# Performance work log

Hardware: AMD Instinct MI355X
Metric: run time of the kernel (lower is better)

The kernel has to match this reference:

```python
import jax, jax.numpy as jnp
import numpy as np

N, D, E = 16384, 256, 131072  # nodes, feature dim, directed edges (avg sym degree ~16)


def _build_graph(rng):
    # random edges with no self-loops
    r = rng.integers(0, N, E)
    c = (r + 1 + rng.integers(0, N - 1, E)) % N
    e = np.stack([r, c], 1)
    # symmetrize + dedupe + sort == torch sparse coalesce()
    e = np.unique(np.concatenate([e, e[:, ::-1]], 0), axis=0)
    rows, cols = e[:, 0], e[:, 1]
    deg = np.bincount(rows, minlength=N)
    max_deg = int(deg.max())
    off = np.concatenate([[0], np.cumsum(deg)])
    pos = np.arange(rows.shape[0]) - off[rows]
    nbr = np.zeros((N, max_deg), dtype=np.int32)  # padded neighbor lists (CSR rows)
    nbr[rows, pos] = cols
    return nbr, deg.astype(np.int32)


def setup_inputs() -> dict:
    rng = np.random.default_rng(0)
    vertices = jnp.asarray(rng.standard_normal((N, D)).astype(np.float32))
    nbr, deg = _build_graph(rng)
    return {"vertices": vertices, "nbr": jnp.asarray(nbr), "deg": jnp.asarray(deg)}


def _compute_means(vertices, nbr, deg):
    # Sequential greedy edge-based vertex averaging (RelEdgePool phase 1).
    n, d = vertices.shape
    max_deg = nbr.shape[1]
    slot = jnp.arange(max_deg)

    def step(carry, xs):
        unproc, out, c = carry
        i, nbrs_i, deg_i = xs
        valid = slot < deg_i                      # real (non-pad) neighbors
        sel = valid & unproc[nbrs_i]              # unprocessed cluster members (excl. self)
        is_head = unproc[i]                       # vertex starts a new valid cluster
        # mean over unprocessed members; self is always included when head
        s = jnp.einsum('kd,k->d', vertices[nbrs_i], sel.astype(vertices.dtype)) + vertices[i]
        cnt = (jnp.sum(sel) + 1).astype(vertices.dtype)
        mean = s / cnt
        out = out.at[c].set(jnp.where(is_head, mean, out[c]))
        # mark selected members (and self) as processed, only if this is a head
        mark = jnp.zeros(n, bool).at[nbrs_i].max(sel).at[i].set(True)
        unproc = unproc & ~(mark & is_head)
        c = c + is_head.astype(c.dtype)
        return (unproc, out, c), is_head

    init = (jnp.ones(n, dtype=bool), jnp.zeros((n, d), vertices.dtype), jnp.int32(0))
    (_, out, num_clusters), head_mask = jax.lax.scan(
        step, init, (jnp.arange(n), nbr, deg))
    # out[:num_clusters] are the averaged vertices; rows beyond are zero (preallocated buffer,
    # matching the torch code before its final data-dependent slice).
    # head_mask marks vertex_mappings; mean_mappings == arange(num_clusters).
    return out, head_mask, num_clusters


def reference(vertices, nbr, deg):
    return _compute_means(vertices, nbr, deg)
```

## Files before the change

kernel.cpp:

```cpp
#include <hip/hip_runtime.h>
#include <cstdint>
#include <cstddef>

#define NV 16384
#define DD 256
#define BLK 1024
#define PCAP 7
#define HROW 24

__global__ __launch_bounds__(256)
void k_prep(const int* __restrict__ nbr, const int* __restrict__ deg,
            int maxdeg, int n, uint4* __restrict__ pend_g,
            unsigned short* __restrict__ hi_g)
{
    int v = blockIdx.x * 256 + threadIdx.x;
    if (v >= n) return;
    const int b  = v & ~(BLK - 1);
    const int dv = deg[v];
    const int* __restrict__ row = nbr + (size_t)v * (size_t)maxdeg;
    unsigned short* __restrict__ hrow = hi_g + (size_t)v * HROW;
    unsigned w0 = 0, w1 = 0, w2 = 0, w3 = 0;
    int cnt = 0, hic = 0;
    for (int k = 0; k < dv; ++k) {
        int j = row[k];
        if (j > v) {
            if (hic < HROW - 1) hrow[1 + hic] = (unsigned short)j;
            ++hic;
        } else if (j >= b) {
            unsigned val = (unsigned)(j - b);
            switch (cnt) {
                case 0: w0 |= val << 16; break;
                case 1: w1 |= val;       break;
                case 2: w1 |= val << 16; break;
                case 3: w2 |= val;       break;
                case 4: w2 |= val << 16; break;
                case 5: w3 |= val;       break;
                case 6: w3 |= val << 16; break;
                default: break;
            }
            ++cnt;
        }
    }
    hrow[0] = (unsigned short)hic;
    w0 |= (unsigned)(cnt > 0xffff ? 0xffff : cnt);
    uint4 p; p.x = w0; p.y = w1; p.z = w2; p.w = w3;
    pend_g[v] = p;
}

__global__ __launch_bounds__(1024)
void k_mis(const int* __restrict__ nbr, const int* __restrict__ deg,
           int maxdeg, int n,
           const uint4* __restrict__ pend_g, const unsigned short* __restrict__ hi_g,
           int* __restrict__ headlist, float* __restrict__ out_tail)
{
    __shared__ __align__(16) unsigned char st[NV];
    __shared__ int s_ws[16];
    __shared__ int F[3];
    const int t    = threadIdx.x;
    const int lane = t & 63;
    const int wid  = t >> 6;

    ((uint4*)st)[t] = make_uint4(0u, 0u, 0u, 0u);
    if (t < 3) F[t] = 0;
    __syncthreads();

    uint4 pv = make_uint4(0,0,0,0), h0 = pv, h1 = pv, h2 = pv;
    int   dv = 0;
    if (t < n) {
        pv = pend_g[t];
        const uint4* hp = (const uint4*)(hi_g + (size_t)t * HROW);
        h0 = hp[0]; h1 = hp[1]; h2 = hp[2];
        dv = deg[t];
    }
    int r = 0;

    for (int b = 0; b < n; b += BLK) {
        const int v = b + t;
        uint4 pn = make_uint4(0,0,0,0), n0 = pn, n1 = pn, n2 = pn;
        int   dn = 0;
        {
            int vn = b + BLK + t;
            if (vn < n) {
                pn = pend_g[vn];
                const uint4* hp = (const uint4*)(hi_g + (size_t)vn * HROW);
                n0 = hp[0]; n1 = hp[1]; n2 = hp[2];
                dn = deg[vn];
            }
        }

        const int np = pv.x & 0xffff;
        const int e0 = pv.x >> 16,    e1 = pv.y & 0xffff, e2 = pv.y >> 16;
        const int e3 = pv.z & 0xffff, e4 = pv.z >> 16;
        const int e5 = pv.w & 0xffff, e6 = pv.w >> 16;
        const int hic = (int)(h0.x & 0xffff);
        const int* __restrict__ row = nbr + (size_t)v * (size_t)maxdeg;

        int my = (v < n) ? 0 : 2;
        for (;; ++r) {
            if (t == 0) F[(r + 1) % 3] = 0;
            #pragma unroll
            for (int pass = 0; pass < 3; ++pass) {
                if (my == 0) {
                    if (st[v] != 0) { my = 2; }
                    else {
                        bool anyH = false; int undec = 0;
                        if (np <= PCAP) {
                            if (np > 0) { int s = st[b + e0]; anyH |= (s == 1); undec += (s == 0); }
                            if (np > 1) { int s = st[b + e1]; anyH |= (s == 1); undec += (s == 0); }
                            if (np > 2) { int s = st[b + e2]; anyH |= (s == 1); undec += (s == 0); }
                            if (np > 3) { int s = st[b + e3]; anyH |= (s == 1); undec += (s == 0); }
                            if (np > 4) { int s = st[b + e4]; anyH |= (s == 1); undec += (s == 0); }
                            if (np > 5) { int s = st[b + e5]; anyH |= (s == 1); undec += (s == 0); }
                            if (np > 6) { int s = st[b + e6]; anyH |= (s == 1); undec += (s == 0); }
                        } else {
                            for (int k = 0; k < dv; ++k) {
                                int j = row[k];
                                if (j >= b && j < v) {
                                    int s = st[j];
                                    anyH |= (s == 1); undec += (s == 0);
                                }
                            }
                        }
                        if (anyH) { my = 2; }
                        else if (undec == 0) {
                            my = 1;
                            st[v] = 1;
                            if (hic <= HROW - 1) {
                                #define PUSHE(word, sh, i) if ((i) < hic) st[((word) >> (sh)) & 0xffffu] = 2
                                PUSHE(h0.x,16, 0); PUSHE(h0.y, 0, 1); PUSHE(h0.y,16, 2);
                                PUSHE(h0.z, 0, 3); PUSHE(h0.z,16, 4); PUSHE(h0.w, 0, 5);
                                PUSHE(h0.w,16, 6);
                                PUSHE(h1.x, 0, 7); PUSHE(h1.x,16, 8); PUSHE(h1.y, 0, 9);
                                PUSHE(h1.y,16,10); PUSHE(h1.z, 0,11); PUSHE(h1.z,16,12);
                                PUSHE(h1.w, 0,13); PUSHE(h1.w,16,14);
                                PUSHE(h2.x, 0,15); PUSHE(h2.x,16,16); PUSHE(h2.y, 0,17);
                                PUSHE(h2.y,16,18); PUSHE(h2.z, 0,19); PUSHE(h2.z,16,20);
                                PUSHE(h2.w, 0,21); PUSHE(h2.w,16,22);
                                #undef PUSHE
                            } else {
                                for (int k = 0; k < dv; ++k) {
                                    int j = row[k];
                                    if (j > v) st[j] = 2;
                                }
                            }
                        }
                    }
                }
            }
            if (my == 0) F[r % 3] = 1;
            __syncthreads();
            if (F[r % 3] == 0) { ++r; break; }
        }
        pv = pn; h0 = n0; h1 = n1; h2 = n2; dv = dn;
    }

    const int base = t * (NV / 1024);
    int cnt = 0;
    #pragma unroll
    for (int i = 0; i < NV / 1024; ++i) {
        int v = base + i;
        cnt += (v < n && st[v] == 1) ? 1 : 0;
    }
    int c = cnt;
    #pragma unroll
    for (int off = 1; off < 64; off <<= 1) {
        int x = __shfl_up(c, off);
        if (lane >= off) c += x;
    }
    if (lane == 63) s_ws[wid] = c;
    __syncthreads();
    int wexcl = 0, tot = 0;
    #pragma unroll
    for (int w = 0; w < 16; ++w) {
        int s = s_ws[w];
        tot += s;
        if (w < wid) wexcl += s;
    }
    int excl = wexcl + (c - cnt);
    #pragma unroll
    for (int i = 0; i < NV / 1024; ++i) {
        int v = base + i;
        if (v < n && st[v] == 1) { headlist[excl] = v; ++excl; }
    }
    for (int i = t; i < n; i += 1024)
        out_tail[i] = (st[i] == 1) ? 1.0f : 0.0f;
    if (t == 0) out_tail[n] = (float)tot;
}

__global__ __launch_bounds__(256)
void k_owner(const int* __restrict__ nbr, const int* __restrict__ deg,
             int maxdeg, int n,
             const float* __restrict__ hm, int* __restrict__ owner)
{
    int gid = blockIdx.x * 256 + threadIdx.x;
    int v = gid >> 4, l = gid & 15;
    if (v >= n) return;
    if (hm[v] != 0.0f) { if (l == 0) owner[v] = v; return; }
    const int* __restrict__ row = nbr + (size_t)v * (size_t)maxdeg;
    const int dv = deg[v];
    int mn = 0x7fffffff;
    for (int k = l; k < dv; k += 16) {
        int j = row[k];
        if (hm[j] != 0.0f) mn = min(mn, j);
    }
    #pragma unroll
    for (int off = 8; off; off >>= 1) mn = min(mn, __shfl_xor(mn, off, 16));
    if (l == 0) owner[v] = mn;
}

__global__ __launch_bounds__(256)
void k_avg(const float* __restrict__ vert, const int* __restrict__ nbr,
           const int* __restrict__ deg, int maxdeg, int n,
           const int* __restrict__ headlist, const int* __restrict__ owner,
           const float* __restrict__ tail, float* __restrict__ out)
{
    const int w    = (blockIdx.x * 256 + threadIdx.x) >> 6;
    const int lane = threadIdx.x & 63;
    const int tot  = (int)tail[n];
    if (w >= tot) return;
    const int h = headlist[w];

    const int dh = deg[h];
    const int* __restrict__ row = nbr + (size_t)h * (size_t)maxdeg;

    float4 acc = reinterpret_cast<const float4*>(vert + (size_t)h * DD)[lane];
    int cnt = 1;

    for (int k0 = 0; k0 < dh; k0 += 64) {
        int k = k0 + lane;
        int j = (k < dh) ? row[k] : -1;
        bool mem = (j >= 0) && (owner[j] == h);
        unsigned long long m = __ballot(mem);
        cnt += __popcll(m);
        while (m) {
            int bit = __ffsll((long long)m) - 1;
            m &= (m - 1);
            int jj = __shfl(j, bit);
            float4 rr = reinterpret_cast<const float4*>(vert + (size_t)jj * DD)[lane];
            acc.x += rr.x; acc.y += rr.y; acc.z += rr.z; acc.w += rr.w;
        }
    }
    const float inv = 1.0f / (float)cnt;
    float4 res;
    res.x = acc.x * inv; res.y = acc.y * inv;
    res.z = acc.z * inv; res.w = acc.w * inv;
    reinterpret_cast<float4*>(out + (size_t)w * DD)[lane] = res;
}

extern "C" void kernel_launch(void* const* d_in, const int* in_sizes, int n_in,
                              void* d_out, int out_size, void* d_ws, size_t ws_size,
                              hipStream_t stream)
{
    const float* vert = (const float*)d_in[0];
    const int*   nbr  = (const int*)d_in[1];
    const int*   deg  = (const int*)d_in[2];

    const int n      = in_sizes[2];
    const int maxdeg = in_sizes[1] / n;
    const int d      = in_sizes[0] / n;

    int*   owner    = (int*)d_ws;
    int*   headlist = owner + n;
    uint4* pend_g   = (uint4*)(headlist + n);
    unsigned short* hi_g = (unsigned short*)(pend_g + n);

    float* out      = (float*)d_out;
    float* out_tail = out + (size_t)n * (size_t)d;

    hipMemsetAsync(d_out, 0, (size_t)out_size * sizeof(float), stream);

    hipLaunchKernelGGL(k_prep, dim3((n + 255) / 256), dim3(256), 0, stream,
                       nbr, deg, maxdeg, n, pend_g, hi_g);

    hipLaunchKernelGGL(k_mis, dim3(1), dim3(1024), 0, stream,
                       nbr, deg, maxdeg, n, pend_g, hi_g, headlist, out_tail);

    hipLaunchKernelGGL(k_owner, dim3((n * 16 + 255) / 256), dim3(256), 0, stream,
                       nbr, deg, maxdeg, n, out_tail, owner);

    const int blocks = (n * 64 + 255) / 256;
    hipLaunchKernelGGL(k_avg, dim3(blocks), dim3(256), 0, stream,
                       vert, nbr, deg, maxdeg, n, headlist, owner, out_tail, out);
}
```

Measured before the change: 89.08 us.

## Cut MIS barriers with wave-early-exit passes and fold owner search into averaging

The MIS loop now runs up to eight inner passes per barrier, using volatile shared-memory reads so updates from other waves become visible and a wavefront ballot to leave early. It marks vertices dominated by a head and replaces __syncthreads with a raw s_barrier. The separate owner kernel and the full-output memset are removed. Instead, k_avg recomputes each candidate neighbor's minimum head on the fly and zero-fills the unused output rows itself. The head-list compaction and the tail float writes are vectorised over packed bytes. This trades fewer launches and barriers for redundant neighbor scans inside k_avg.

Result: no change. 87.39 us (-1.9%).

```diff
diff --git a/kernel.cpp b/kernel.cpp
--- a/kernel.cpp
+++ b/kernel.cpp
@@ -4,9 +4,13 @@
 
 #define NV 16384
 #define DD 256
+#define TPB 1024
 #define BLK 1024
 #define PCAP 7
 #define HROW 24
+#define NPASS 8
+
+#define VST(P, IDX) ((int)*((volatile const unsigned char*)(P) + (IDX)))
 
 __global__ __launch_bounds__(256)
 void k_prep(const int* __restrict__ nbr, const int* __restrict__ deg,
@@ -43,18 +47,17 @@
     }
     hrow[0] = (unsigned short)hic;
     w0 |= (unsigned)(cnt > 0xffff ? 0xffff : cnt);
-    uint4 p; p.x = w0; p.y = w1; p.z = w2; p.w = w3;
-    pend_g[v] = p;
-}
-
-__global__ __launch_bounds__(1024)
+    pend_g[v] = make_uint4(w0, w1, w2, w3);
+}
+
+__global__ __launch_bounds__(TPB, 4)
 void k_mis(const int* __restrict__ nbr, const int* __restrict__ deg,
            int maxdeg, int n,
            const uint4* __restrict__ pend_g, const unsigned short* __restrict__ hi_g,
            int* __restrict__ headlist, float* __restrict__ out_tail)
 {
     __shared__ __align__(16) unsigned char st[NV];
-    __shared__ int s_ws[16];
+    __shared__ int s_ws[TPB / 64];
     __shared__ int F[3];
     const int t    = threadIdx.x;
     const int lane = t & 63;
@@ -98,35 +101,38 @@
         int my = (v < n) ? 0 : 2;
         for (;; ++r) {
             if (t == 0) F[(r + 1) % 3] = 0;
-            #pragma unroll
-            for (int pass = 0; pass < 3; ++pass) {
+            for (int pass = 0; pass < NPASS; ++pass) {
                 if (my == 0) {
-                    if (st[v] != 0) { my = 2; }
+                    if (VST(st, v) != 0) { my = 2; }
                     else {
                         bool anyH = false; int undec = 0;
                         if (np <= PCAP) {
-                            if (np > 0) { int s = st[b + e0]; anyH |= (s == 1); undec += (s == 0); }
-                            if (np > 1) { int s = st[b + e1]; anyH |= (s == 1); undec += (s == 0); }
-                            if (np > 2) { int s = st[b + e2]; anyH |= (s == 1); undec += (s == 0); }
-                            if (np > 3) { int s = st[b + e3]; anyH |= (s == 1); undec += (s == 0); }
-                            if (np > 4) { int s = st[b + e4]; anyH |= (s == 1); undec += (s == 0); }
-                            if (np > 5) { int s = st[b + e5]; anyH |= (s == 1); undec += (s == 0); }
-                            if (np > 6) { int s = st[b + e6]; anyH |= (s == 1); undec += (s == 0); }
+                            int q0 = VST(st, b + e0), q1 = VST(st, b + e1);
+                            int q2 = VST(st, b + e2), q3 = VST(st, b + e3);
+                            int q4 = VST(st, b + e4), q5 = VST(st, b + e5);
+                            int q6 = VST(st, b + e6);
+                            if (np > 0) { anyH |= (q0 == 1); undec += (q0 == 0); }
+                            if (np > 1) { anyH |= (q1 == 1); undec += (q1 == 0); }
+                            if (np > 2) { anyH |= (q2 == 1); undec += (q2 == 0); }
+                            if (np > 3) { anyH |= (q3 == 1); undec += (q3 == 0); }
+                            if (np > 4) { anyH |= (q4 == 1); undec += (q4 == 0); }
+                            if (np > 5) { anyH |= (q5 == 1); undec += (q5 == 0); }
+                            if (np > 6) { anyH |= (q6 == 1); undec += (q6 == 0); }
                         } else {
                             for (int k = 0; k < dv; ++k) {
                                 int j = row[k];
                                 if (j >= b && j < v) {
-                                    int s = st[j];
-                                    anyH |= (s == 1); undec += (s == 0);
+                                    int q = VST(st, j);
+                                    anyH |= (q == 1); undec += (q == 0);
                                 }
                             }
                         }
-                        if (anyH) { my = 2; }
+                        if (anyH) { my = 2; st[v] = 2; }
                         else if (undec == 0) {
                             my = 1;
                             st[v] = 1;
                             if (hic <= HROW - 1) {
-                                #define PUSHE(word, sh, i) if ((i) < hic) st[((word) >> (sh)) & 0xffffu] = 2
+                                #define PUSHE(word, sh, k) if ((k) < hic) st[((word) >> (sh)) & 0xffffu] = 2
                                 PUSHE(h0.x,16, 0); PUSHE(h0.y, 0, 1); PUSHE(h0.y,16, 2);
                                 PUSHE(h0.z, 0, 3); PUSHE(h0.z,16, 4); PUSHE(h0.w, 0, 5);
                                 PUSHE(h0.w,16, 6);
@@ -146,21 +152,18 @@
                         }
                     }
                 }
+                if (__ballot(my == 0) == 0ULL) break;
             }
             if (my == 0) F[r % 3] = 1;
-            __syncthreads();
+            asm volatile("s_waitcnt lgkmcnt(0)\n\ts_barrier" ::: "memory");
             if (F[r % 3] == 0) { ++r; break; }
         }
         pv = pn; h0 = n0; h1 = n1; h2 = n2; dv = dn;
     }
 
-    const int base = t * (NV / 1024);
-    int cnt = 0;
-    #pragma unroll
-    for (int i = 0; i < NV / 1024; ++i) {
-        int v = base + i;
-        cnt += (v < n && st[v] == 1) ? 1 : 0;
-    }
+    uint4 qq = ((const uint4*)st)[t];
+    int cnt = __popc(qq.x & 0x01010101u) + __popc(qq.y & 0x01010101u)
+            + __popc(qq.z & 0x01010101u) + __popc(qq.w & 0x01010101u);
     int c = cnt;
     #pragma unroll
     for (int off = 1; off < 64; off <<= 1) {
@@ -171,53 +174,41 @@
     __syncthreads();
     int wexcl = 0, tot = 0;
     #pragma unroll
-    for (int w = 0; w < 16; ++w) {
+    for (int w = 0; w < TPB / 64; ++w) {
         int s = s_ws[w];
         tot += s;
         if (w < wid) wexcl += s;
     }
     int excl = wexcl + (c - cnt);
     #pragma unroll
-    for (int i = 0; i < NV / 1024; ++i) {
-        int v = base + i;
-        if (v < n && st[v] == 1) { headlist[excl] = v; ++excl; }
-    }
-    for (int i = t; i < n; i += 1024)
-        out_tail[i] = (st[i] == 1) ? 1.0f : 0.0f;
+    for (int i = 0; i < 16; ++i) {
+        int v = t * 16 + i;
+        if (st[v] == 1) { headlist[excl] = v; ++excl; }
+    }
+    for (int i = t; i < NV / 4; i += TPB) {
+        unsigned w = ((const unsigned*)st)[i];
+        float4 f;
+        f.x = (float)(w & 1u);         f.y = (float)((w >> 8) & 1u);
+        f.z = (float)((w >> 16) & 1u); f.w = (float)((w >> 24) & 1u);
+        ((float4*)out_tail)[i] = f;
+    }
     if (t == 0) out_tail[n] = (float)tot;
-}
-
-__global__ __launch_bounds__(256)
-void k_owner(const int* __restrict__ nbr, const int* __restrict__ deg,
-             int maxdeg, int n,
-             const float* __restrict__ hm, int* __restrict__ owner)
-{
-    int gid = blockIdx.x * 256 + threadIdx.x;
-    int v = gid >> 4, l = gid & 15;
-    if (v >= n) return;
-    if (hm[v] != 0.0f) { if (l == 0) owner[v] = v; return; }
-    const int* __restrict__ row = nbr + (size_t)v * (size_t)maxdeg;
-    const int dv = deg[v];
-    int mn = 0x7fffffff;
-    for (int k = l; k < dv; k += 16) {
-        int j = row[k];
-        if (hm[j] != 0.0f) mn = min(mn, j);
-    }
-    #pragma unroll
-    for (int off = 8; off; off >>= 1) mn = min(mn, __shfl_xor(mn, off, 16));
-    if (l == 0) owner[v] = mn;
 }
 
 __global__ __launch_bounds__(256)
 void k_avg(const float* __restrict__ vert, const int* __restrict__ nbr,
            const int* __restrict__ deg, int maxdeg, int n,
-           const int* __restrict__ headlist, const int* __restrict__ owner,
+           const int* __restrict__ headlist,
            const float* __restrict__ tail, float* __restrict__ out)
 {
     const int w    = (blockIdx.x * 256 + threadIdx.x) >> 6;
     const int lane = threadIdx.x & 63;
+    if (w >= n) return;
     const int tot  = (int)tail[n];
-    if (w >= tot) return;
+    if (w >= tot) {
+        reinterpret_cast<float4*>(out + (size_t)w * DD)[lane] = make_float4(0.f, 0.f, 0.f, 0.f);
+        return;
+    }
     const int h = headlist[w];
 
     const int dh = deg[h];
@@ -229,7 +220,17 @@
     for (int k0 = 0; k0 < dh; k0 += 64) {
         int k = k0 + lane;
         int j = (k < dh) ? row[k] : -1;
-        bool mem = (j >= 0) && (owner[j] == h);
+        bool mem = false;
+        if (j > h && tail[j] == 0.0f) {
+            const int dj = deg[j];
+            const int* __restrict__ rj = nbr + (size_t)j * (size_t)maxdeg;
+            int mn = 0x7fffffff;
+            for (int kk = 0; kk < dj; ++kk) {
+                int u = rj[kk];
+                if (tail[u] != 0.0f) mn = min(mn, u);
+            }
+            mem = (mn == h);
+        }
         unsigned long long m = __ballot(mem);
         cnt += __popcll(m);
         while (m) {
@@ -259,26 +260,20 @@
     const int maxdeg = in_sizes[1] / n;
     const int d      = in_sizes[0] / n;
 
-    int*   owner    = (int*)d_ws;
-    int*   headlist = owner + n;
+    int*   headlist = (int*)d_ws;
     uint4* pend_g   = (uint4*)(headlist + n);
     unsigned short* hi_g = (unsigned short*)(pend_g + n);
 
     float* out      = (float*)d_out;
     float* out_tail = out + (size_t)n * (size_t)d;
 
-    hipMemsetAsync(d_out, 0, (size_t)out_size * sizeof(float), stream);
-
     hipLaunchKernelGGL(k_prep, dim3((n + 255) / 256), dim3(256), 0, stream,
                        nbr, deg, maxdeg, n, pend_g, hi_g);
 
-    hipLaunchKernelGGL(k_mis, dim3(1), dim3(1024), 0, stream,
+    hipLaunchKernelGGL(k_mis, dim3(1), dim3(TPB), 0, stream,
                        nbr, deg, maxdeg, n, pend_g, hi_g, headlist, out_tail);
-
-    hipLaunchKernelGGL(k_owner, dim3((n * 16 + 255) / 256), dim3(256), 0, stream,
-                       nbr, deg, maxdeg, n, out_tail, owner);
 
     const int blocks = (n * 64 + 255) / 256;
     hipLaunchKernelGGL(k_avg, dim3(blocks), dim3(256), 0, stream,
-                       vert, nbr, deg, maxdeg, n, headlist, owner, out_tail, out);
-}
+                       vert, nbr, deg, maxdeg, n, headlist, out_tail, out);
+}
```
